# Performance work log

Hardware: AMD Instinct MI355X
Metric: run time of the kernel (lower is better)

## Reference

```python
import jax, jax.numpy as jnp
import numpy as np

# DeltaNet single-token decode step. Hard-coded dims from the torch source:
# hidden H=2048 (chosen), qk=2048 (16h x 128 -> repeat to 32h), v=4096 (32h x 128),
# conv channels 8192, kernel 4, state [1,32,128,128].
H = 2048
EPS = 1e-6

def _l2norm(x):
    return x * jax.lax.rsqrt(jnp.sum(x * x, axis=-1, keepdims=True) + EPS)

def setup_inputs() -> dict:
    key = jax.random.key(0)
    ks = jax.random.split(key, 12)
    w = lambda k, s, sc=0.02: jax.random.normal(k, s, dtype=jnp.float32) * sc
    return {
        "x": jax.random.normal(ks[0], (1, 1, H), dtype=jnp.float32),
        "state": jax.random.normal(ks[1], (1, 32, 128, 128), dtype=jnp.float32) * 0.02,
        "conv_state": jax.random.normal(ks[2], (1, 8192, 3), dtype=jnp.float32) * 0.1,
        "W_qkv": w(ks[3], (8192, H)),
        "W_z": w(ks[4], (4096, H)),
        "W_b": w(ks[5], (32, H)),
        "W_a": w(ks[6], (32, H)),
        "conv_w": w(ks[7], (8192, 1, 4), 0.3),
        "A_log": jax.random.uniform(ks[8], (32,), minval=-2.0, maxval=0.0, dtype=jnp.float32),
        "dt_bias": w(ks[9], (32,), 0.5),
        "norm_w": jnp.ones((128,), jnp.float32),
        "W_out": w(ks[10], (H, 4096)),
    }

def reference(x, state, conv_state, W_qkv, W_z, W_b, W_a, conv_w, A_log, dt_bias, norm_w, W_out):
    # projections (bias-free Linear, torch convention y = x @ W.T)
    mixed = jnp.einsum('blh,ch->blc', x, W_qkv)           # [1,1,8192]
    z = jnp.einsum('blh,ch->blc', x, W_z).reshape(1, 1, 32, 128)
    beta = jax.nn.sigmoid(jnp.einsum('blh,ch->blc', x, W_b))  # [1,1,32]
    a = jnp.einsum('blh,ch->blc', x, W_a)                 # [1,1,32]

    # depthwise causal conv (groups=8192, kernel 4, output length 1)
    combined = jnp.concatenate([conv_state, mixed.transpose(0, 2, 1)], axis=-1)  # [1,8192,4]
    new_conv = combined[:, :, -3:]
    conv_out = jnp.sum(combined * conv_w[None, :, 0, :], axis=-1)  # [1,8192]
    mixed = jax.nn.silu(conv_out)[:, None, :]             # [1,1,8192]

    q, k, v = mixed[..., :2048], mixed[..., 2048:4096], mixed[..., 4096:]
    q = jnp.repeat(q.reshape(1, 1, 16, 128), 2, axis=2)   # [1,1,32,128]
    k = jnp.repeat(k.reshape(1, 1, 16, 128), 2, axis=2)
    v = v.reshape(1, 1, 32, 128)

    g = -jnp.exp(A_log) * jax.nn.softplus(a + dt_bias)    # [1,1,32]

    q = _l2norm(q)[:, 0] / jnp.sqrt(jnp.float32(128.0))   # [1,32,128]
    k = _l2norm(k)[:, 0]
    v = v[:, 0]
    g_t = jnp.exp(g[:, 0])[..., None, None]               # [1,32,1,1]
    beta_t = beta[:, 0][..., None]                        # [1,32,1]

    # gated delta-rule state update
    s = state * g_t                                       # [1,32,128,128]
    kv_mem = jnp.einsum('bhkv,bhk->bhv', s, k)            # [1,32,128]
    delta = (v - kv_mem) * beta_t
    new_state = s + k[..., None] * delta[..., None, :]    # [1,32,128,128]
    out = jnp.einsum('bhkv,bhk->bhv', new_state, q)       # [1,32,128]

    # gated RMSNorm (Mamba2-style: rmsnorm(x * silu(z)) * w)
    out_flat = out.reshape(-1, 128)
    z_flat = z.reshape(-1, 128)
    gated = out_flat * jax.nn.silu(z_flat)
    out_flat = gated * jax.lax.rsqrt(jnp.mean(gated * gated, axis=-1, keepdims=True) + EPS) * norm_w

    out = jnp.einsum('blc,hc->blh', out_flat.reshape(1, 1, 4096), W_out)  # [1,1,H]
    return (out, new_state, new_conv)
```

## Files before the change

### kernel.cpp

```cpp
#include <hip/hip_runtime.h>
#include <hip/hip_cooperative_groups.h>
#include <math.h>

namespace cg = cooperative_groups;

__device__ __forceinline__ float silu(float x){ return x / (1.f + expf(-x)); }

__device__ __forceinline__ void gemv_in_pairs(
    int pairIdx, int pairStride, int lane,
    const float* __restrict__ x,
    const float* __restrict__ W_qkv, const float* __restrict__ W_z,
    const float* __restrict__ W_b,   const float* __restrict__ W_a,
    float* __restrict__ mixed, float* __restrict__ zb,
    float* __restrict__ b_raw, float* __restrict__ a_raw)
{
  float4 xr[8];
  #pragma unroll
  for (int j = 0; j < 8; j++)
    xr[j] = *(const float4*)(x + j*256 + lane*4);

  for (int rp = pairIdx; rp < 6176; rp += pairStride){
    const int row0 = rp * 2;
    const float* W; float* dst;
    if (row0 < 8192)       { W = W_qkv + (size_t)row0 * 2048;          dst = mixed + row0; }
    else if (row0 < 12288) { W = W_z   + (size_t)(row0-8192) * 2048;   dst = zb + (row0-8192); }
    else if (row0 < 12320) { W = W_b   + (size_t)(row0-12288) * 2048;  dst = b_raw + (row0-12288); }
    else                   { W = W_a   + (size_t)(row0-12320) * 2048;  dst = a_raw + (row0-12320); }

    float acc0 = 0.f, acc1 = 0.f;
    #pragma unroll
    for (int j = 0; j < 8; j++){
      float4 w0 = *(const float4*)(W + j*256 + lane*4);
      float4 w1 = *(const float4*)(W + 2048 + j*256 + lane*4);
      acc0 += w0.x*xr[j].x + w0.y*xr[j].y + w0.z*xr[j].z + w0.w*xr[j].w;
      acc1 += w1.x*xr[j].x + w1.y*xr[j].y + w1.z*xr[j].z + w1.w*xr[j].w;
    }
    #pragma unroll
    for (int off = 32; off >= 1; off >>= 1){
      acc0 += __shfl_xor(acc0, off, 64);
      acc1 += __shfl_xor(acc1, off, 64);
    }
    if (lane == 0){ dst[0] = acc0; dst[1] = acc1; }
  }
}

struct HeadSmem {
  float qn[128];
  float kn[128];
  __align__(16) float vs[128];
  float4 kvp[8][32];
  float red[4];
};

__device__ __forceinline__ void head_work(
    int h, int tid, HeadSmem& sm,
    const float* __restrict__ mixed,      const float* __restrict__ conv_state,
    const float* __restrict__ conv_w,     const float* __restrict__ zbuf,
    const float* __restrict__ b_raw,      const float* __restrict__ a_raw,
    const float* __restrict__ A_log,      const float* __restrict__ dt_bias,
    const float* __restrict__ norm_w,     const float* __restrict__ state,
    float* __restrict__ new_state, float* __restrict__ new_conv,
    float* __restrict__ out_flat)
{
  const int hb = h >> 1;
  const int t  = tid & 127;
  const int lane = tid & 63, wid = tid >> 6;

  float qv = 0.f, kv = 0.f;
  if (tid < 128){
    int c = hb*128 + t;
    float c0 = conv_state[c*3+0], c1 = conv_state[c*3+1], c2 = conv_state[c*3+2];
    float m  = mixed[c];
    qv = silu(c0*conv_w[c*4+0] + c1*conv_w[c*4+1] + c2*conv_w[c*4+2] + m*conv_w[c*4+3]);
    new_conv[c*3+0] = c1; new_conv[c*3+1] = c2; new_conv[c*3+2] = m;
    c = 2048 + hb*128 + t;
    c0 = conv_state[c*3+0]; c1 = conv_state[c*3+1]; c2 = conv_state[c*3+2];
    m  = mixed[c];
    kv = silu(c0*conv_w[c*4+0] + c1*conv_w[c*4+1] + c2*conv_w[c*4+2] + m*conv_w[c*4+3]);
    new_conv[c*3+0] = c1; new_conv[c*3+1] = c2; new_conv[c*3+2] = m;

    float sq = qv*qv, sk = kv*kv;
    #pragma unroll
    for (int off = 32; off >= 1; off >>= 1){
      sq += __shfl_xor(sq, off, 64);
      sk += __shfl_xor(sk, off, 64);
    }
    if (lane == 0){ sm.red[wid] = sq; sm.red[2+wid] = sk; }
  } else {
    int c = 4096 + h*128 + t;
    float c0 = conv_state[c*3+0], c1 = conv_state[c*3+1], c2 = conv_state[c*3+2];
    float m  = mixed[c];
    sm.vs[t] = silu(c0*conv_w[c*4+0] + c1*conv_w[c*4+1] + c2*conv_w[c*4+2] + m*conv_w[c*4+3]);
    new_conv[c*3+0] = c1; new_conv[c*3+1] = c2; new_conv[c*3+2] = m;
  }
  __syncthreads();
  const float qscale = rsqrtf(sm.red[0]+sm.red[1] + 1e-6f) * 0.088388347648318440550f;
  const float kscale = rsqrtf(sm.red[2]+sm.red[3] + 1e-6f);
  if (tid < 128){ sm.qn[t] = qv * qscale; sm.kn[t] = kv * kscale; }
  __syncthreads();

  float g_t, beta;
  {
    const float av = a_raw[h] + dt_bias[h];
    const float sp = (av > 20.f) ? av : log1pf(expf(av));
    g_t  = expf(-expf(A_log[h]) * sp);
    beta = 1.f / (1.f + expf(-b_raw[h]));
  }

  const int cg_ = tid & 31, part = tid >> 5;
  const int k0 = part * 16;
  const float* st  = state     + (size_t)h * 16384;
  float*       nst = new_state + (size_t)h * 16384;

  float4 s4[16];
  float4 kvm = make_float4(0.f, 0.f, 0.f, 0.f);
  #pragma unroll
  for (int i = 0; i < 16; i++){
    float4 sv = *(const float4*)(st + (k0+i)*128 + cg_*4);
    sv.x *= g_t; sv.y *= g_t; sv.z *= g_t; sv.w *= g_t;
    s4[i] = sv;
    const float kk = sm.kn[k0+i];
    kvm.x += sv.x*kk; kvm.y += sv.y*kk; kvm.z += sv.z*kk; kvm.w += sv.w*kk;
  }
  sm.kvp[part][cg_] = kvm;
  __syncthreads();
  float4 kt = make_float4(0.f, 0.f, 0.f, 0.f);
  #pragma unroll
  for (int p = 0; p < 8; p++){
    float4 kp = sm.kvp[p][cg_];
    kt.x += kp.x; kt.y += kp.y; kt.z += kp.z; kt.w += kp.w;
  }
  const float4 v4 = *(const float4*)(sm.vs + cg_*4);
  float4 delta;
  delta.x = (v4.x - kt.x) * beta;
  delta.y = (v4.y - kt.y) * beta;
  delta.z = (v4.z - kt.z) * beta;
  delta.w = (v4.w - kt.w) * beta;

  float4 oacc = make_float4(0.f, 0.f, 0.f, 0.f);
  #pragma unroll
  for (int i = 0; i < 16; i++){
    const float kk = sm.kn[k0+i];
    float4 ns;
    ns.x = s4[i].x + kk*delta.x;
    ns.y = s4[i].y + kk*delta.y;
    ns.z = s4[i].z + kk*delta.z;
    ns.w = s4[i].w + kk*delta.w;
    *(float4*)(nst + (k0+i)*128 + cg_*4) = ns;
    const float qq = sm.qn[k0+i];
    oacc.x += ns.x*qq; oacc.y += ns.y*qq; oacc.z += ns.z*qq; oacc.w += ns.w*qq;
  }
  __syncthreads();
  sm.kvp[part][cg_] = oacc;
  __syncthreads();
  if (part == 0){
    float4 o = make_float4(0.f, 0.f, 0.f, 0.f);
    #pragma unroll
    for (int p = 0; p < 8; p++){
      float4 op = sm.kvp[p][cg_];
      o.x += op.x; o.y += op.y; o.z += op.z; o.w += op.w;
    }
    const float4 z4 = *(const float4*)(zbuf + h*128 + cg_*4);
    float4 g4;
    g4.x = o.x * silu(z4.x);
    g4.y = o.y * silu(z4.y);
    g4.z = o.z * silu(z4.z);
    g4.w = o.w * silu(z4.w);
    float s2 = g4.x*g4.x + g4.y*g4.y + g4.z*g4.z + g4.w*g4.w;
    #pragma unroll
    for (int off = 16; off >= 1; off >>= 1) s2 += __shfl_xor(s2, off, 64);
    const float r = rsqrtf(s2 * (1.f/128.f) + 1e-6f);
    const float4 nw = *(const float4*)(norm_w + cg_*4);
    float4 ov;
    ov.x = g4.x * r * nw.x;
    ov.y = g4.y * r * nw.y;
    ov.z = g4.z * r * nw.z;
    ov.w = g4.w * r * nw.w;
    *(float4*)(out_flat + h*128 + cg_*4) = ov;
  }
}

__global__ __launch_bounds__(256, 4) void k_fused(
    const float* __restrict__ x,
    const float* __restrict__ conv_state,
    const float* __restrict__ W_qkv,
    const float* __restrict__ W_z,
    const float* __restrict__ W_b,
    const float* __restrict__ W_a,
    const float* __restrict__ conv_w,
    const float* __restrict__ A_log,
    const float* __restrict__ dt_bias,
    const float* __restrict__ norm_w,
    const float* __restrict__ state,
    const float* __restrict__ Wout,
    float* __restrict__ out,
    float* __restrict__ new_state,
    float* __restrict__ new_conv,
    float* __restrict__ mixed,
    float* __restrict__ zb,
    float* __restrict__ b_raw,
    float* __restrict__ a_raw,
    float* __restrict__ oflat,
    float* __restrict__ scratch)
{
  cg::grid_group grid = cg::this_grid();
  const int b    = blockIdx.x;
  const int tid  = threadIdx.x;
  const int lane = tid & 63;
  const int wave = tid >> 6;

  __shared__ HeadSmem sm;
  __shared__ __align__(16) float xs[4096];
  __shared__ float redC[4];

  gemv_in_pairs(b*4 + wave, 4096, lane, x, W_qkv, W_z, W_b, W_a,
                mixed, zb, b_raw, a_raw);

  grid.sync();

  if (b < 32){
    head_work(b, tid, sm, mixed, conv_state, conv_w, zb, b_raw, a_raw,
              A_log, dt_bias, norm_w, state, new_state, new_conv, oflat);
  } else {
    const float4* W4 = (const float4*)Wout + (size_t)b * 2048;
    float4 a = make_float4(0.f, 0.f, 0.f, 0.f);
    #pragma unroll
    for (int j = 0; j < 8; j++){
      float4 w = W4[j*256 + tid];
      a.x += w.x; a.y += w.y; a.z += w.z; a.w += w.w;
    }
    if (b >= 992){
      const float4* W2 = (const float4*)Wout + (size_t)(b-992) * 2048;
      #pragma unroll
      for (int j = 0; j < 8; j++){
        float4 w = W2[j*256 + tid];
        a.x += w.x; a.y += w.y; a.z += w.z; a.w += w.w;
      }
    }
    if (tid == 0) scratch[b] = a.x + a.y + a.z + a.w;
  }

  grid.sync();

  #pragma unroll
  for (int i = 0; i < 4; i++)
    *(float4*)(xs + tid*4 + i*1024) = *(const float4*)(oflat + tid*4 + i*1024);
  __syncthreads();

  const int row  = b*2 + (wave >> 1);
  const int half = wave & 1;
  const float* Wr = Wout + (size_t)row * 4096 + half * 2048;
  const float* xh = xs + half * 2048;
  float acc = 0.f;
  #pragma unroll
  for (int j = 0; j < 8; j++){
    float4 w = *(const float4*)(Wr + j*256 + lane*4);
    acc += w.x*xh[j*256+lane*4+0] + w.y*xh[j*256+lane*4+1]
         + w.z*xh[j*256+lane*4+2] + w.w*xh[j*256+lane*4+3];
  }
  #pragma unroll
  for (int off = 32; off >= 1; off >>= 1) acc += __shfl_xor(acc, off, 64);
  if (lane == 0) redC[wave] = acc;
  __syncthreads();
  if (tid < 2) out[b*2 + tid] = redC[2*tid] + redC[2*tid+1];
}

__global__ __launch_bounds__(256) void k_gemv_in(
    const float* __restrict__ x,
    const float* __restrict__ W_qkv, const float* __restrict__ W_z,
    const float* __restrict__ W_b,   const float* __restrict__ W_a,
    float* __restrict__ mixed, float* __restrict__ zb,
    float* __restrict__ b_raw, float* __restrict__ a_raw)
{
  const int lane = threadIdx.x & 63, wave = threadIdx.x >> 6;
  gemv_in_pairs(blockIdx.x*4 + wave, 6176, lane, x, W_qkv, W_z, W_b, W_a,
                mixed, zb, b_raw, a_raw);
}

__global__ __launch_bounds__(256) void k_head(
    const float* __restrict__ mixed,      const float* __restrict__ conv_state,
    const float* __restrict__ conv_w,     const float* __restrict__ zbuf,
    const float* __restrict__ b_raw,      const float* __restrict__ a_raw,
    const float* __restrict__ A_log,      const float* __restrict__ dt_bias,
    const float* __restrict__ norm_w,     const float* __restrict__ state,
    const float* __restrict__ Wout,
    float* __restrict__ new_state, float* __restrict__ new_conv,
    float* __restrict__ out_flat,  float* __restrict__ scratch)
{
  const int b = blockIdx.x, tid = threadIdx.x;
  if (b >= 32){
    const float4* W4 = (const float4*)Wout + (size_t)b * 8192;
    float4 a = make_float4(0.f, 0.f, 0.f, 0.f);
    #pragma unroll
    for (int j = 0; j < 32; j++){
      float4 w = W4[j*256 + tid];
      a.x += w.x; a.y += w.y; a.z += w.z; a.w += w.w;
    }
    if (tid == 0) scratch[b] = a.x + a.y + a.z + a.w;
    return;
  }
  __shared__ HeadSmem sm;
  head_work(b, tid, sm, mixed, conv_state, conv_w, zbuf, b_raw, a_raw,
            A_log, dt_bias, norm_w, state, new_state, new_conv, out_flat);
}

__global__ __launch_bounds__(256) void k_gemv_out(
    const float* __restrict__ out_flat,
    const float* __restrict__ Wout,
    float* __restrict__ out)
{
  __shared__ __align__(16) float xs[4096];
  const int tid = threadIdx.x;
  #pragma unroll
  for (int i = 0; i < 4; i++)
    *(float4*)(xs + tid*4 + i*1024) = *(const float4*)(out_flat + tid*4 + i*1024);
  __syncthreads();

  const int lane = tid & 63, wave = tid >> 6;
  const int row0 = blockIdx.x * 8 + wave * 2;
  const float* W0 = Wout + (size_t)row0 * 4096;
  float acc0 = 0.f, acc1 = 0.f;
  #pragma unroll
  for (int j = 0; j < 16; j++){
    float4 w0 = *(const float4*)(W0 + j*256 + lane*4);
    float4 w1 = *(const float4*)(W0 + 4096 + j*256 + lane*4);
    const float x0 = xs[j*256+lane*4+0], x1 = xs[j*256+lane*4+1];
    const float x2 = xs[j*256+lane*4+2], x3 = xs[j*256+lane*4+3];
    acc0 += w0.x*x0 + w0.y*x1 + w0.z*x2 + w0.w*x3;
    acc1 += w1.x*x0 + w1.y*x1 + w1.z*x2 + w1.w*x3;
  }
  #pragma unroll
  for (int off = 32; off >= 1; off >>= 1){
    acc0 += __shfl_xor(acc0, off, 64);
    acc1 += __shfl_xor(acc1, off, 64);
  }
  if (lane == 0){ out[row0] = acc0; out[row0+1] = acc1; }
}

extern "C" void kernel_launch(void* const* d_in, const int* in_sizes, int n_in,
                              void* d_out, int out_size, void* d_ws, size_t ws_size,
                              hipStream_t stream) {
  const float* x          = (const float*)d_in[0];
  const float* state      = (const float*)d_in[1];
  const float* conv_state = (const float*)d_in[2];
  const float* W_qkv      = (const float*)d_in[3];
  const float* W_z        = (const float*)d_in[4];
  const float* W_b        = (const float*)d_in[5];
  const float* W_a        = (const float*)d_in[6];
  const float* conv_w     = (const float*)d_in[7];
  const float* A_log      = (const float*)d_in[8];
  const float* dt_bias    = (const float*)d_in[9];
  const float* norm_w     = (const float*)d_in[10];
  const float* W_out      = (const float*)d_in[11];

  float* out       = (float*)d_out;
  float* new_state = (float*)d_out + 2048;
  float* new_conv  = (float*)d_out + 2048 + 524288;

  float* ws      = (float*)d_ws;
  float* mixed   = ws;
  float* zb      = ws + 8192;
  float* b_raw   = ws + 12288;
  float* a_raw   = ws + 12320;
  float* oflat   = ws + 12352;
  float* scratch = ws + 16448;

  int maxBlk = 0;
  hipError_t qe = hipOccupancyMaxActiveBlocksPerMultiprocessor(
      &maxBlk, (const void*)k_fused, 256, 0);
  bool coop_ok = (qe == hipSuccess && maxBlk >= 4);

  if (coop_ok){
    void* args[] = {
      (void*)&x, (void*)&conv_state, (void*)&W_qkv, (void*)&W_z, (void*)&W_b,
      (void*)&W_a, (void*)&conv_w, (void*)&A_log, (void*)&dt_bias, (void*)&norm_w,
      (void*)&state, (void*)&W_out,
      (void*)&out, (void*)&new_state, (void*)&new_conv,
      (void*)&mixed, (void*)&zb, (void*)&b_raw, (void*)&a_raw, (void*)&oflat,
      (void*)&scratch
    };
    hipError_t le = hipLaunchCooperativeKernel((const void*)k_fused,
                                               dim3(1024), dim3(256),
                                               args, 0, stream);
    if (le == hipSuccess) return;
  }

  hipLaunchKernelGGL(k_gemv_in, dim3(1544), dim3(256), 0, stream,
                     x, W_qkv, W_z, W_b, W_a, mixed, zb, b_raw, a_raw);
  hipLaunchKernelGGL(k_head, dim3(256), dim3(256), 0, stream,
                     mixed, conv_state, conv_w, zb, b_raw, a_raw, A_log, dt_bias,
                     norm_w, state, W_out, new_state, new_conv, oflat, scratch);
  hipLaunchKernelGGL(k_gemv_out, dim3(256), dim3(256), 0, stream,
                     oflat, W_out, out);
}
```

Baseline: 179.5 us.

## Prefetch W_out rows into registers during head phase, drop L2 warm-up

Blocks that are idle during the per-head delta-rule phase now load their W_out row slices straight into registers, and the head blocks load theirs after head work, all before the second grid sync. This replaces the earlier dummy sum-reduce that only warmed the cache with W_out. After the sync, the output GEMV reads oflat from global memory and multiplies by the register-held weights, so the shared-memory staging of oflat and its block barrier go away. The cost is 32 extra VGPRs per thread, and oflat is now read from global memory by every wave.

```diff
diff --git a/kernel.cpp b/kernel.cpp
--- a/kernel.cpp
+++ b/kernel.cpp
@@ -200,8 +200,7 @@
     float* __restrict__ zb,
     float* __restrict__ b_raw,
     float* __restrict__ a_raw,
-    float* __restrict__ oflat,
-    float* __restrict__ scratch)
+    float* __restrict__ oflat)
 {
   cg::grid_group grid = cg::this_grid();
   const int b    = blockIdx.x;
@@ -210,7 +209,6 @@
   const int wave = tid >> 6;
 
   __shared__ HeadSmem sm;
-  __shared__ __align__(16) float xs[4096];
   __shared__ float redC[4];
 
   gemv_in_pairs(b*4 + wave, 4096, lane, x, W_qkv, W_z, W_b, W_a,
@@ -218,51 +216,39 @@
 
   grid.sync();
 
+  const int rowC = b*2 + (wave >> 1);
+  const int half = wave & 1;
+  const float* Wr = Wout + (size_t)rowC * 4096 + half * 2048;
+
+  float4 wreg[8];
   if (b < 32){
     head_work(b, tid, sm, mixed, conv_state, conv_w, zb, b_raw, a_raw,
               A_log, dt_bias, norm_w, state, new_state, new_conv, oflat);
+    #pragma unroll
+    for (int j = 0; j < 8; j++)
+      wreg[j] = *(const float4*)(Wr + j*256 + lane*4);
   } else {
-    const float4* W4 = (const float4*)Wout + (size_t)b * 2048;
-    float4 a = make_float4(0.f, 0.f, 0.f, 0.f);
+    #pragma unroll
+    for (int j = 0; j < 8; j++)
+      wreg[j] = *(const float4*)(Wr + j*256 + lane*4);
+  }
+
+  grid.sync();
+
+  {
+    const float* xh = oflat + half * 2048;
+    float acc = 0.f;
     #pragma unroll
     for (int j = 0; j < 8; j++){
-      float4 w = W4[j*256 + tid];
-      a.x += w.x; a.y += w.y; a.z += w.z; a.w += w.w;
-    }
-    if (b >= 992){
-      const float4* W2 = (const float4*)Wout + (size_t)(b-992) * 2048;
-      #pragma unroll
-      for (int j = 0; j < 8; j++){
-        float4 w = W2[j*256 + tid];
-        a.x += w.x; a.y += w.y; a.z += w.z; a.w += w.w;
-      }
-    }
-    if (tid == 0) scratch[b] = a.x + a.y + a.z + a.w;
-  }
-
-  grid.sync();
-
-  #pragma unroll
-  for (int i = 0; i < 4; i++)
-    *(float4*)(xs + tid*4 + i*1024) = *(const float4*)(oflat + tid*4 + i*1024);
-  __syncthreads();
-
-  const int row  = b*2 + (wave >> 1);
-  const int half = wave & 1;
-  const float* Wr = Wout + (size_t)row * 4096 + half * 2048;
-  const float* xh = xs + half * 2048;
-  float acc = 0.f;
-  #pragma unroll
-  for (int j = 0; j < 8; j++){
-    float4 w = *(const float4*)(Wr + j*256 + lane*4);
-    acc += w.x*xh[j*256+lane*4+0] + w.y*xh[j*256+lane*4+1]
-         + w.z*xh[j*256+lane*4+2] + w.w*xh[j*256+lane*4+3];
-  }
-  #pragma unroll
-  for (int off = 32; off >= 1; off >>= 1) acc += __shfl_xor(acc, off, 64);
-  if (lane == 0) redC[wave] = acc;
-  __syncthreads();
-  if (tid < 2) out[b*2 + tid] = redC[2*tid] + redC[2*tid+1];
+      float4 xv = *(const float4*)(xh + j*256 + lane*4);
+      acc += wreg[j].x*xv.x + wreg[j].y*xv.y + wreg[j].z*xv.z + wreg[j].w*xv.w;
+    }
+    #pragma unroll
+    for (int off = 32; off >= 1; off >>= 1) acc += __shfl_xor(acc, off, 64);
+    if (lane == 0) redC[wave] = acc;
+    __syncthreads();
+    if (tid < 2) out[b*2 + tid] = redC[2*tid] + redC[2*tid+1];
+  }
 }
 
 __global__ __launch_bounds__(256) void k_gemv_in(
@@ -376,8 +362,7 @@
       (void*)&W_a, (void*)&conv_w, (void*)&A_log, (void*)&dt_bias, (void*)&norm_w,
       (void*)&state, (void*)&W_out,
       (void*)&out, (void*)&new_state, (void*)&new_conv,
-      (void*)&mixed, (void*)&zb, (void*)&b_raw, (void*)&a_raw, (void*)&oflat,
-      (void*)&scratch
+      (void*)&mixed, (void*)&zb, (void*)&b_raw, (void*)&a_raw, (void*)&oflat
     };
     hipError_t le = hipLaunchCooperativeKernel((const void*)k_fused,
                                                dim3(1024), dim3(256),
```

Result: no change. 177.6 us (-1.0%).
